# Kernel tuning notes

Hardware: AMD Instinct MI355X
Metric: run time of the kernel (lower is better)

Reference implementation:

```python
import jax, jax.numpy as jnp
import numpy as np


def _relative_index(ih: int, iw: int) -> np.ndarray:
    # Static precompute mirroring the torch buffer.
    yy, xx = np.meshgrid(np.arange(ih), np.arange(iw), indexing='ij')
    coords = np.stack([yy.ravel(), xx.ravel()])                 # [2, n]
    rel = coords[:, :, None] - coords[:, None, :]               # [2, n, n]
    rel[0] += ih - 1
    rel[1] += iw - 1
    rel[0] *= 2 * iw - 1
    return rel.sum(0).ravel()                                   # [n*n]


def setup_inputs() -> dict:
    key = jax.random.key(0)
    ks = jax.random.split(key, 5)
    B, N, INP, OUP, HEADS = 64, 256, 512, 512, 16
    ih = iw = 16
    return {
        'x': jax.random.normal(ks[0], (B, N, INP), jnp.float32),
        'w_qkv': jax.random.normal(ks[1], (INP, 3 * OUP), jnp.float32) * 0.02,
        'rel_bias_table': jax.random.normal(ks[2], ((2 * ih - 1) * (2 * iw - 1), HEADS), jnp.float32) * 0.02,
        'w_out': jax.random.normal(ks[3], (OUP, OUP), jnp.float32) * 0.02,
        'b_out': jax.random.normal(ks[4], (OUP,), jnp.float32) * 0.02,
        'ih': ih,
        'iw': iw,
    }


def reference(x, w_qkv, rel_bias_table, w_out, b_out, ih, iw):
    B, N, _ = x.shape
    heads = rel_bias_table.shape[1]
    oup = w_out.shape[0]
    dim_head = oup // heads
    scale = dim_head ** -0.5

    qkv = jnp.einsum('bni,ij->bnj', x, w_qkv)                   # [B, N, 3*oup]
    q, k, v = jnp.split(qkv, 3, axis=-1)
    split_heads = lambda t: t.reshape(B, N, heads, dim_head).transpose(0, 2, 1, 3)
    q, k, v = split_heads(q), split_heads(k), split_heads(v)    # [B, H, N, D]

    dots = jnp.einsum('bhnd,bhmd->bhnm', q, k) * scale          # [B, H, N, N]
    rel_idx = jnp.asarray(_relative_index(int(ih), int(iw)))    # [N*N]
    bias = rel_bias_table[rel_idx].reshape(N, N, heads)         # gather
    dots = dots + bias.transpose(2, 0, 1)[None]                 # [1, H, N, N]

    attn = jax.nn.softmax(dots, axis=-1)
    out = jnp.einsum('bhnm,bhmd->bhnd', attn, v)                # [B, H, N, D]
    out = out.transpose(0, 2, 1, 3).reshape(B, N, oup)
    return jnp.einsum('bno,op->bnp', out, w_out.T) + b_out
```

## Files before the change

kernel.cpp:

```cpp
#include <hip/hip_runtime.h>
#include <stdint.h>

typedef unsigned short u16;
typedef unsigned int u32;
typedef __attribute__((ext_vector_type(8))) __bf16 bf16x8;
typedef __attribute__((ext_vector_type(2))) u32 u32x2;
typedef __attribute__((ext_vector_type(4))) u32 u32x4;
typedef __attribute__((ext_vector_type(4))) float f32x4;

__device__ __forceinline__ float bf2f(u16 x) { return __uint_as_float(((u32)x) << 16); }
__device__ __forceinline__ u16 f2bf(float f) {
  u32 u = __float_as_uint(f);
  u32 r = (u + 0x7fffu + ((u >> 16) & 1u)) >> 16;
  return (u16)r;
}
__device__ __forceinline__ u16 cvbf(float f) {
  union { __bf16 b; u16 u; } x;
  x.b = (__bf16)f;
  return x.u;
}

__device__ __forceinline__ u32x2 ld8(const u16* p) { return *(const u32x2*)p; }
__device__ __forceinline__ u32x4 ld16(const u16* p) { return *(const u32x4*)p; }
__device__ __forceinline__ bf16x8 mk_frag(u32x2 lo, u32x2 hi) {
  union { bf16x8 v; u32x2 u[2]; } t;
  t.u[0] = lo; t.u[1] = hi;
  return t.v;
}

__device__ __forceinline__ void g2l16(const void* g, void* l) {
  __builtin_amdgcn_global_load_lds(
      (const __attribute__((address_space(1))) u32*)g,
      (__attribute__((address_space(3))) u32*)l, 16, 0, 0);
}

__device__ __forceinline__ void stage_fm(u16* lds, int ch, u32x4 v) {
  int row = ch >> 2, q = ch & 3;
  *(u32x4*)&lds[(row >> 4) * 512 + q * 128 + (row & 15) * 8] = v;
}

__device__ __forceinline__ bf16x8 frag_fm(const u16* lds, int subtile, int g, int c) {
  union { bf16x8 v; u32x4 u; } t;
  t.u = ld16(&lds[subtile * 512 + g * 128 + c * 8]);
  return t.v;
}

__global__ void probe_dtype(const u32* __restrict__ x, u32* __restrict__ flag) {
  if (threadIdx.x == 0 && blockIdx.x == 0) {
    int cnt = 0;
    for (int i = 0; i < 32; ++i) {
      u32 e = (x[i] >> 7) & 0xffu;
      cnt += (e >= 96u && e <= 140u) ? 1 : 0;
    }
    *flag = (cnt == 32) ? 1u : 0u;
  }
}

__global__ __launch_bounds__(256) void conv4(const void* __restrict__ src, u16* __restrict__ dst,
                                             const u32* __restrict__ flag, int n4) {
  const bool isbf = (*flag != 0u);
  const int stride = gridDim.x * 256;
  for (int i = blockIdx.x * 256 + threadIdx.x; i < n4; i += stride) {
    if (isbf) {
      ((u32x2*)dst)[i] = ((const u32x2*)src)[i];
    } else {
      const float* s = (const float*)src + (size_t)i * 4;
      u32x2 o;
      o.x = (u32)f2bf(s[0]) | ((u32)f2bf(s[1]) << 16);
      o.y = (u32)f2bf(s[2]) | ((u32)f2bf(s[3]) << 16);
      ((u32x2*)dst)[i] = o;
    }
  }
}

__global__ __launch_bounds__(256) void bias_prep(const void* __restrict__ table,
                                                 float* __restrict__ biasT,
                                                 const u32* __restrict__ flag) {
  const bool isbf = (*flag != 0u);
  int i = blockIdx.x * 256 + threadIdx.x;
  if (i < 16 * 961) {
    int h = i / 961, idx = i - h * 961;
    float v = isbf ? bf2f(((const u16*)table)[idx * 16 + h])
                   : ((const float*)table)[idx * 16 + h];
    biasT[i] = v * 1.4426950408889634f;
  }
}

__global__ __launch_bounds__(256) void transpose_dt(const void* __restrict__ in,
                                                    u16* __restrict__ out,
                                                    const u32* __restrict__ flag, int R, int C) {
  __shared__ u16 t[32][33];
  const bool isbf = (*flag != 0u);
  int r0 = blockIdx.y * 32, c0 = blockIdx.x * 32;
  int rr = threadIdx.x >> 5, cc = threadIdx.x & 31;
#pragma unroll
  for (int i = 0; i < 4; ++i) {
    size_t idx = (size_t)(r0 + rr + i * 8) * C + c0 + cc;
    t[rr + i * 8][cc] = isbf ? ((const u16*)in)[idx] : f2bf(((const float*)in)[idx]);
  }
  __syncthreads();
#pragma unroll
  for (int i = 0; i < 4; ++i) out[(size_t)(c0 + rr + i * 8) * R + r0 + cc] = t[cc][rr + i * 8];
}

__global__ __launch_bounds__(256) void gemm128(const u16* __restrict__ A,
                                               const u16* __restrict__ BT,
                                               u16* __restrict__ O, int K, int ldo) {
  __shared__ u16 As[128 * 32];
  __shared__ u16 Bs[128 * 32];
  const int tid = threadIdx.x;
  const int wave = tid >> 6, lane = tid & 63;
  const int c = lane & 15, g = lane >> 4;
  const int wm = wave >> 1, wn = wave & 1;
  const int bn = blockIdx.x, bm = blockIdx.y;

  const u16* Ab = A + (size_t)bm * 128 * K;
  const u16* Bb = BT + (size_t)bn * 128 * K;

  const u16* Arow = Ab + (size_t)(wave * 16 + c) * K + 8 * g;
  const u16* Brow = Bb + (size_t)(wave * 16 + c) * K + 8 * g;
  u16* Ad0 = &As[wave * 512 + lane * 8];
  u16* Ad1 = &As[(wave + 4) * 512 + lane * 8];
  u16* Bd0 = &Bs[wave * 512 + lane * 8];
  u16* Bd1 = &Bs[(wave + 4) * 512 + lane * 8];

  f32x4 acc[4][4] = {};

  for (int k0 = 0; k0 < K; k0 += 32) {
    g2l16(Arow + k0, Ad0);
    g2l16(Arow + 64 * K + k0, Ad1);
    g2l16(Brow + k0, Bd0);
    g2l16(Brow + 64 * K + k0, Bd1);
    __syncthreads();
    bf16x8 af[4], bfr[4];
#pragma unroll
    for (int i = 0; i < 4; ++i) {
      af[i] = frag_fm(As, wm * 4 + i, g, c);
      bfr[i] = frag_fm(Bs, wn * 4 + i, g, c);
    }
#pragma unroll
    for (int i = 0; i < 4; ++i)
#pragma unroll
      for (int j = 0; j < 4; ++j)
        acc[i][j] = __builtin_amdgcn_mfma_f32_16x16x32_bf16(af[i], bfr[j], acc[i][j], 0, 0, 0);
    __syncthreads();
  }

#pragma unroll
  for (int i = 0; i < 4; ++i)
#pragma unroll
    for (int j = 0; j < 4; ++j) {
      int jg = bn * 128 + wn * 64 + j * 16 + c;
#pragma unroll
      for (int r = 0; r < 4; ++r) {
        int mg = bm * 128 + wm * 64 + i * 16 + 4 * g + r;
        O[(size_t)mg * ldo + jg] = f2bf(acc[i][j][r]);
      }
    }
}

__global__ __launch_bounds__(256) void gemm_final(const u16* __restrict__ A,
                                                  const u16* __restrict__ BT,
                                                  const u16* __restrict__ bias,
                                                  void* __restrict__ O, int row0g,
                                                  const u32* __restrict__ flag) {
  __shared__ u16 As[128 * 32];
  __shared__ u16 Bs[128 * 32];
  const int K = 512;
  const bool isbf = (*flag != 0u);
  const int tid = threadIdx.x;
  const int wave = tid >> 6, lane = tid & 63;
  const int c = lane & 15, g = lane >> 4;
  const int wm = wave >> 1, wn = wave & 1;
  const int bn = blockIdx.x, bm = blockIdx.y;

  const u16* Ab = A + (size_t)bm * 128 * K;
  const u16* Bb = BT + (size_t)bn * 128 * K;

  const u16* Arow = Ab + (size_t)(wave * 16 + c) * K + 8 * g;
  const u16* Brow = Bb + (size_t)(wave * 16 + c) * K + 8 * g;
  u16* Ad0 = &As[wave * 512 + lane * 8];
  u16* Ad1 = &As[(wave + 4) * 512 + lane * 8];
  u16* Bd0 = &Bs[wave * 512 + lane * 8];
  u16* Bd1 = &Bs[(wave + 4) * 512 + lane * 8];

  f32x4 acc[4][4] = {};

  for (int k0 = 0; k0 < K; k0 += 32) {
    g2l16(Arow + k0, Ad0);
    g2l16(Arow + 64 * K + k0, Ad1);
    g2l16(Brow + k0, Bd0);
    g2l16(Brow + 64 * K + k0, Bd1);
    __syncthreads();
    bf16x8 af[4], bfr[4];
#pragma unroll
    for (int i = 0; i < 4; ++i) {
      af[i] = frag_fm(As, wm * 4 + i, g, c);
      bfr[i] = frag_fm(Bs, wn * 4 + i, g, c);
    }
#pragma unroll
    for (int i = 0; i < 4; ++i)
#pragma unroll
      for (int j = 0; j < 4; ++j)
        acc[i][j] = __builtin_amdgcn_mfma_f32_16x16x32_bf16(af[i], bfr[j], acc[i][j], 0, 0, 0);
    __syncthreads();
  }

#pragma unroll
  for (int i = 0; i < 4; ++i)
#pragma unroll
    for (int j = 0; j < 4; ++j) {
      int jg = bn * 128 + wn * 64 + j * 16 + c;
      float bv = bf2f(bias[jg]);
#pragma unroll
      for (int r = 0; r < 4; ++r) {
        int mg = bm * 128 + wm * 64 + i * 16 + 4 * g + r;
        float v = acc[i][j][r] + bv;
        size_t off = (size_t)(row0g + mg) * 512 + jg;
        if (isbf) ((u16*)O)[off] = f2bf(v);
        else ((float*)O)[off] = v;
      }
    }
}

__global__ __launch_bounds__(256) void attn_kernel(const u16* __restrict__ qkv,
                                                   const float* __restrict__ biasT,
                                                   u16* __restrict__ Out) {
  __shared__ u16 smem[18432];
  float* biasS = (float*)&smem[16384];

  const int tid = threadIdx.x;
  const int wave = tid >> 6, lane = tid & 63;
  const int c = lane & 15, g = lane >> 4;
  const int half = blockIdx.x & 1;
  const int h = (blockIdx.x >> 1) & 15;
  const int b = blockIdx.x >> 5;

  const u16* xb = qkv + (size_t)b * 256 * 1536;

  u32x4 kvr[4];
#pragma unroll
  for (int i = 0; i < 4; ++i) {
    int ch = tid + i * 256;
    int m = ch >> 2;
    kvr[i] = ld16(xb + (size_t)m * 1536 + 512 + h * 32 + (ch & 3) * 8);
  }
#pragma unroll
  for (int i = 0; i < 4; ++i) stage_fm(smem, tid + i * 256, kvr[i]);

#pragma unroll
  for (int i = 0; i < 16; ++i) {
    int e2 = tid + i * 256;
    int n = e2 >> 4, d = (e2 & 15) * 2;
    u32 val = *(const u32*)(xb + (size_t)n * 1536 + 1024 + h * 32 + d);
    smem[8192 + d * 256 + (n ^ (8 * (d & 7)))] = (u16)(val & 0xffffu);
    smem[8192 + (d + 1) * 256 + (n ^ (8 * ((d + 1) & 7)))] = (u16)(val >> 16);
  }
  for (int i = tid; i < 961; i += 256) biasS[i] = biasT[h * 961 + i];

  u32x4 qv[2];
#pragma unroll
  for (int rg = 0; rg < 2; ++rg) {
    const u16* qp = xb + (size_t)((half * 2 + rg) * 64 + wave * 16 + c) * 1536 + h * 32 + 8 * g;
    qv[rg] = ld16(qp);
  }
  __syncthreads();

  const u16* Vt = &smem[8192];
  const int va = 8 * (c & 7);
  const float scale2 = 0.25503484f;
  const float* bp0 = biasS + wave * 31 + c + 12 - 4 * g;

#pragma unroll
  for (int rg = 0; rg < 2; ++rg) {
    const int rgg = half * 2 + rg;
    union { bf16x8 v; u32x4 u; } qt;
    qt.u = qv[rg];
    bf16x8 qf = qt.v;

    f32x4 o0 = {0.f, 0.f, 0.f, 0.f}, o1 = {0.f, 0.f, 0.f, 0.f};
    float smm = 0.f;

#pragma unroll
    for (int ph = 0; ph < 2; ++ph) {
      f32x4 s[8];
#pragma unroll
      for (int f = 0; f < 8; ++f) {
        bf16x8 kf = frag_fm(smem, ph * 8 + f, g, c);
        f32x4 z = {0.f, 0.f, 0.f, 0.f};
        s[f] = __builtin_amdgcn_mfma_f32_16x16x32_bf16(kf, qf, z, 0, 0, 0);
      }

      float u[8];
#pragma unroll
      for (int f = 0; f < 8; ++f) {
        const int fg = ph * 8 + f;
#pragma unroll
        for (int j = 0; j < 4; ++j) {
          float bv = bp0[(rgg * 4 - fg + 15) * 31 + 3 - j];
          s[f][j] = __builtin_amdgcn_exp2f(s[f][j] * scale2 + bv);
        }
        u[f] = (s[f][0] + s[f][1]) + (s[f][2] + s[f][3]);
      }
      smm += ((u[0] + u[4]) + (u[1] + u[5])) + ((u[2] + u[6]) + (u[3] + u[7]));

#pragma unroll
      for (int q = 0; q < 4; ++q) {
        bf16x8 pf;
        pf[0] = (__bf16)s[2 * q][0]; pf[1] = (__bf16)s[2 * q][1];
        pf[2] = (__bf16)s[2 * q][2]; pf[3] = (__bf16)s[2 * q][3];
        pf[4] = (__bf16)s[2 * q + 1][0]; pf[5] = (__bf16)s[2 * q + 1][1];
        pf[6] = (__bf16)s[2 * q + 1][2]; pf[7] = (__bf16)s[2 * q + 1][3];
        const int kg = (ph * 4 + q) * 32;
        bf16x8 v0 = mk_frag(ld8(&Vt[c * 256 + ((kg + 4 * g) ^ va)]),
                            ld8(&Vt[c * 256 + ((kg + 16 + 4 * g) ^ va)]));
        bf16x8 v1 = mk_frag(ld8(&Vt[(16 + c) * 256 + ((kg + 4 * g) ^ va)]),
                            ld8(&Vt[(16 + c) * 256 + ((kg + 16 + 4 * g) ^ va)]));
        o0 = __builtin_amdgcn_mfma_f32_16x16x32_bf16(pf, v0, o0, 0, 0, 0);
        o1 = __builtin_amdgcn_mfma_f32_16x16x32_bf16(pf, v1, o1, 0, 0, 0);
      }
    }

    smm += __shfl_xor(smm, 16, 64);
    smm += __shfl_xor(smm, 32, 64);
    const float invc = __builtin_amdgcn_rcpf(smm);

    const int nb = rgg * 64 + wave * 16 + 4 * g;
#pragma unroll
    for (int j = 0; j < 4; ++j) {
      int n = nb + j;
      size_t off = ((size_t)b * 256 + n) * 512 + h * 32;
      Out[off + c] = cvbf(o0[j] * invc);
      Out[off + 16 + c] = cvbf(o1[j] * invc);
    }
  }
}

extern "C" void kernel_launch(void* const* d_in, const int* in_sizes, int n_in, void* d_out,
                              int out_size, void* d_ws, size_t ws_size, hipStream_t stream) {
  (void)in_sizes; (void)n_in; (void)out_size;
  const void* x = d_in[0];
  const void* w_qkv = d_in[1];
  const void* table = d_in[2];
  const void* w_out = d_in[3];
  const void* b_out = d_in[4];

  char* ws = (char*)d_ws;
  u32* flag = (u32*)ws;
  u16* xc = (u16*)(ws + 256);
  u16* wqkvT = (u16*)(ws + 16777472);
  float* biasT = (float*)(ws + 18350336);
  u16* woC = (u16*)(ws + 18411840);
  u16* bC = (u16*)(ws + 18936128);
  const size_t DYN = 18937344;
  int CB = 64;
  while (CB > 1 && DYN + (size_t)CB * 1048576 > ws_size) CB >>= 1;
  u16* qkv = (u16*)(ws + DYN);
  u16* att = (u16*)(ws + DYN + (size_t)CB * 786432);

  dim3 blk(256);
  probe_dtype<<<dim3(1), dim3(64), 0, stream>>>((const u32*)x, flag);
  conv4<<<dim3(2048), blk, 0, stream>>>(x, xc, flag, 2097152);
  conv4<<<dim3(256), blk, 0, stream>>>(w_out, woC, flag, 65536);
  conv4<<<dim3(1), blk, 0, stream>>>(b_out, bC, flag, 128);
  bias_prep<<<dim3(61), blk, 0, stream>>>(table, biasT, flag);
  transpose_dt<<<dim3(48, 16), blk, 0, stream>>>(w_qkv, wqkvT, flag, 512, 1536);

  for (int s0 = 0; s0 < 64; s0 += CB) {
    const u16* xcc = xc + (size_t)s0 * 256 * 512;
    gemm128<<<dim3(12, CB * 2), blk, 0, stream>>>(xcc, wqkvT, qkv, 512, 1536);
    attn_kernel<<<dim3(CB * 32), blk, 0, stream>>>(qkv, biasT, att);
    gemm_final<<<dim3(4, CB * 2), blk, 0, stream>>>(att, woC, bC, d_out, s0 * 256, flag);
  }
}
```

Measured before the change: 150.6 us.

## Double-buffer LDS tiles in projection GEMMs to overlap loads with MFMA

The QKV and output projection GEMM kernels now use two LDS buffers per operand. The next K-slice is prefetched with direct global-to-LDS loads while the current slice is consumed by MFMAs, and the two syncthreads per iteration become one vmcnt wait plus a barrier. This is meant to hide global load latency behind compute. LDS use per block doubles, which could lower occupancy. Correctness relies on the g2l16 loads being tracked by vmcnt.

```diff
diff --git a/kernel.cpp b/kernel.cpp
--- a/kernel.cpp
+++ b/kernel.cpp
@@ -106,8 +106,8 @@
 __global__ __launch_bounds__(256) void gemm128(const u16* __restrict__ A,
                                                const u16* __restrict__ BT,
                                                u16* __restrict__ O, int K, int ldo) {
-  __shared__ u16 As[128 * 32];
-  __shared__ u16 Bs[128 * 32];
+  __shared__ u16 As[2][128 * 32];
+  __shared__ u16 Bs[2][128 * 32];
   const int tid = threadIdx.x;
   const int wave = tid >> 6, lane = tid & 63;
   const int c = lane & 15, g = lane >> 4;
@@ -119,32 +119,44 @@
 
   const u16* Arow = Ab + (size_t)(wave * 16 + c) * K + 8 * g;
   const u16* Brow = Bb + (size_t)(wave * 16 + c) * K + 8 * g;
-  u16* Ad0 = &As[wave * 512 + lane * 8];
-  u16* Ad1 = &As[(wave + 4) * 512 + lane * 8];
-  u16* Bd0 = &Bs[wave * 512 + lane * 8];
-  u16* Bd1 = &Bs[(wave + 4) * 512 + lane * 8];
+  const int ldst = wave * 512 + lane * 8;
+
+#define STAGE_G(buf, k0)                              \
+  do {                                                \
+    g2l16(Arow + (k0), &As[buf][ldst]);               \
+    g2l16(Arow + 64 * K + (k0), &As[buf][2048 + ldst]); \
+    g2l16(Brow + (k0), &Bs[buf][ldst]);               \
+    g2l16(Brow + 64 * K + (k0), &Bs[buf][2048 + ldst]); \
+  } while (0)
 
   f32x4 acc[4][4] = {};
-
-  for (int k0 = 0; k0 < K; k0 += 32) {
-    g2l16(Arow + k0, Ad0);
-    g2l16(Arow + 64 * K + k0, Ad1);
-    g2l16(Brow + k0, Bd0);
-    g2l16(Brow + 64 * K + k0, Bd1);
-    __syncthreads();
+  const int NT = K >> 5;
+
+  STAGE_G(0, 0);
+  asm volatile("s_waitcnt vmcnt(0)" ::: "memory");
+  __builtin_amdgcn_s_barrier();
+  __builtin_amdgcn_sched_barrier(0);
+
+  int cur = 0;
+  for (int t = 0; t < NT; ++t) {
+    if (t + 1 < NT) STAGE_G(cur ^ 1, (t + 1) * 32);
     bf16x8 af[4], bfr[4];
 #pragma unroll
     for (int i = 0; i < 4; ++i) {
-      af[i] = frag_fm(As, wm * 4 + i, g, c);
-      bfr[i] = frag_fm(Bs, wn * 4 + i, g, c);
+      af[i] = frag_fm(&As[cur][0], wm * 4 + i, g, c);
+      bfr[i] = frag_fm(&Bs[cur][0], wn * 4 + i, g, c);
     }
 #pragma unroll
     for (int i = 0; i < 4; ++i)
 #pragma unroll
       for (int j = 0; j < 4; ++j)
         acc[i][j] = __builtin_amdgcn_mfma_f32_16x16x32_bf16(af[i], bfr[j], acc[i][j], 0, 0, 0);
-    __syncthreads();
-  }
+    asm volatile("s_waitcnt vmcnt(0)" ::: "memory");
+    __builtin_amdgcn_s_barrier();
+    __builtin_amdgcn_sched_barrier(0);
+    cur ^= 1;
+  }
+#undef STAGE_G
 
 #pragma unroll
   for (int i = 0; i < 4; ++i)
@@ -164,8 +176,8 @@
                                                   const u16* __restrict__ bias,
                                                   void* __restrict__ O, int row0g,
                                                   const u32* __restrict__ flag) {
-  __shared__ u16 As[128 * 32];
-  __shared__ u16 Bs[128 * 32];
+  __shared__ u16 As[2][128 * 32];
+  __shared__ u16 Bs[2][128 * 32];
   const int K = 512;
   const bool isbf = (*flag != 0u);
   const int tid = threadIdx.x;
@@ -179,32 +191,44 @@
 
   const u16* Arow = Ab + (size_t)(wave * 16 + c) * K + 8 * g;
   const u16* Brow = Bb + (size_t)(wave * 16 + c) * K + 8 * g;
-  u16* Ad0 = &As[wave * 512 + lane * 8];
-  u16* Ad1 = &As[(wave + 4) * 512 + lane * 8];
-  u16* Bd0 = &Bs[wave * 512 + lane * 8];
-  u16* Bd1 = &Bs[(wave + 4) * 512 + lane * 8];
+  const int ldst = wave * 512 + lane * 8;
+
+#define STAGE_G(buf, k0)                              \
+  do {                                                \
+    g2l16(Arow + (k0), &As[buf][ldst]);               \
+    g2l16(Arow + 64 * K + (k0), &As[buf][2048 + ldst]); \
+    g2l16(Brow + (k0), &Bs[buf][ldst]);               \
+    g2l16(Brow + 64 * K + (k0), &Bs[buf][2048 + ldst]); \
+  } while (0)
 
   f32x4 acc[4][4] = {};
-
-  for (int k0 = 0; k0 < K; k0 += 32) {
-    g2l16(Arow + k0, Ad0);
-    g2l16(Arow + 64 * K + k0, Ad1);
-    g2l16(Brow + k0, Bd0);
-    g2l16(Brow + 64 * K + k0, Bd1);
-    __syncthreads();
+  const int NT = K >> 5;
+
+  STAGE_G(0, 0);
+  asm volatile("s_waitcnt vmcnt(0)" ::: "memory");
+  __builtin_amdgcn_s_barrier();
+  __builtin_amdgcn_sched_barrier(0);
+
+  int cur = 0;
+  for (int t = 0; t < NT; ++t) {
+    if (t + 1 < NT) STAGE_G(cur ^ 1, (t + 1) * 32);
     bf16x8 af[4], bfr[4];
 #pragma unroll
     for (int i = 0; i < 4; ++i) {
-      af[i] = frag_fm(As, wm * 4 + i, g, c);
-      bfr[i] = frag_fm(Bs, wn * 4 + i, g, c);
+      af[i] = frag_fm(&As[cur][0], wm * 4 + i, g, c);
+      bfr[i] = frag_fm(&Bs[cur][0], wn * 4 + i, g, c);
     }
 #pragma unroll
     for (int i = 0; i < 4; ++i)
 #pragma unroll
       for (int j = 0; j < 4; ++j)
         acc[i][j] = __builtin_amdgcn_mfma_f32_16x16x32_bf16(af[i], bfr[j], acc[i][j], 0, 0, 0);
-    __syncthreads();
-  }
+    asm volatile("s_waitcnt vmcnt(0)" ::: "memory");
+    __builtin_amdgcn_s_barrier();
+    __builtin_amdgcn_sched_barrier(0);
+    cur ^= 1;
+  }
+#undef STAGE_G
 
 #pragma unroll
   for (int i = 0; i < 4; ++i)
```

After: 152.0 us, median of 2. About the same (+0.9%).
